# Kernel optimization log

Measured on AMD Instinct MI355X. Metric: run time of the kernel, lower is better.

## Reference

```python
import jax, jax.numpy as jnp
import numpy as np

B = 8192      # batch
E = 16        # n_experts
D = 128       # per-expert input dim (equal for all experts)
U = 256       # units
F = 256       # feature_dim (gating input)
G = 4         # n_gates
K = 6         # hard-coded top-k in the original call()
TEMP = 0.01   # hard-coded softmax temperature
LEAKY_SLOPE = 0.2  # keras leaky_relu default negative slope


def setup_inputs() -> dict:
    key = jax.random.key(0)
    ks = jax.random.split(key, 5)
    return {
        "inputs": jax.random.normal(ks[0], (B, E * D), dtype=jnp.float32),
        "feature_input": jax.random.normal(ks[1], (B, F), dtype=jnp.float32),
        # stacked per-expert kernels (equal dims -> one [E, D, U] tensor)
        "expert_kernels": jax.random.normal(ks[2], (E, D, U), dtype=jnp.float32) * 0.05,
        "expert_biases": jnp.zeros((E, U), dtype=jnp.float32),
        "gating_kernels": jax.random.normal(ks[3], (G, F, E), dtype=jnp.float32) * 0.1,
        "gating_biases": jnp.zeros((G, E), dtype=jnp.float32),
        "global_weights": jnp.ones((E,), dtype=jnp.float32),
    }


def reference(inputs, feature_input, expert_kernels, expert_biases,
              gating_kernels, gating_biases, global_weights):
    # ---- per-expert dense + bias + LeakyReLU (tf.split loop -> batched einsum) ----
    x = inputs.reshape(B, E, D)                                   # [B, E, D]
    eo = jnp.einsum('bed,edu->bue', x, expert_kernels)            # [B, U, E]
    eo = eo + expert_biases.T[None, :, :]                         # bias per expert
    expert_outputs = jax.nn.leaky_relu(eo, LEAKY_SLOPE)           # [B, U, E]

    # ---- gating: dense + bias + ReLU, scaled by global_weights ----
    g = jnp.einsum('bf,gfe->bge', feature_input, gating_kernels)  # [B, G, E]
    g = jax.nn.relu(g + gating_biases[None, :, :]) * global_weights

    # sharp softmax over experts, then top-k selection
    p = jax.nn.softmax(g / TEMP, axis=-1)                         # [B, G, E]
    top_v, top_i = jax.lax.top_k(p, K)                            # [B, G, K]

    # gather selected expert outputs: [B, G, U, K]
    sel = jnp.take_along_axis(expert_outputs[:, None, :, :],
                              top_i[:, :, None, :], axis=-1)

    # renormalize top-k values with another sharp softmax, weighted combine
    w = jax.nn.softmax(top_v / TEMP, axis=-1)                     # [B, G, K]
    out = jnp.einsum('bguk,bgk->bgu', sel, w)                     # [B, G, U]
    concat_output = out.reshape(B, G * U)                         # concat over gates
    return concat_output, expert_outputs
```

## Files before the change

### kernel.cpp

```cpp
#include <hip/hip_runtime.h>
#include <stdint.h>

#define NB 8192
#define NE 16
#define ND 128
#define NU 256
#define NF 256
#define NG 4
#define NK 6
#define ITEMP_LOG2E 144.26950408889634f

typedef short short4v __attribute__((ext_vector_type(4)));
typedef short short8v __attribute__((ext_vector_type(8)));
typedef float float4v __attribute__((ext_vector_type(4)));

__device__ __forceinline__ short f2bf(float x) {
  uint32_t u = __builtin_bit_cast(uint32_t, x);
  u += 0x7FFFu + ((u >> 16) & 1u);
  return (short)(u >> 16);
}

__global__ __launch_bounds__(256) void prep_kernel(
    const float* __restrict__ ek,
    short* __restrict__ pb)
{
  int gid = (blockIdx.x << 8) | threadIdx.x;
  int lane = gid & 63, ut = (gid >> 6) & 15, ks = (gid >> 10) & 3, e = gid >> 12;
  int krow = ks * 32 + ((lane >> 4) * 8);
  int ucol = ut * 16 + (lane & 15);
  const float* src = ek + (size_t)(e * 128 + krow) * 256 + ucol;
  short8v v;
#pragma unroll
  for (int j = 0; j < 8; ++j) v[j] = f2bf(src[(size_t)j * 256]);
  *(short8v*)(pb + (size_t)gid * 8) = v;
}

#define APITCH 2056
#define WPITCH 64

__global__ __launch_bounds__(1024, 4) void moe_kernel(
    const float* __restrict__ x,
    const float* __restrict__ feat,
    const float* __restrict__ gk,
    const float* __restrict__ gbias,
    const float* __restrict__ gw,
    const float* __restrict__ eb,
    const short* __restrict__ pb,
    float* __restrict__ out)
{
  __shared__ __align__(16) short ash[32 * APITCH];
  __shared__ __align__(16) float wsh[32 * WPITCH];
  __shared__ __align__(16) float stg[16 * 256];
  int bt = blockIdx.x, tid = threadIdx.x;
  int w = tid >> 6, lane = tid & 63;

  if (w < 14) {
    const float4v* s = (const float4v*)(x + (size_t)bt * 32 * 2048);
    for (int idx = w * 64 + lane; idx < 16384; idx += 896) {
      int row = idx >> 9;
      int colf = (idx & 511) << 2;
      float4v v = __builtin_nontemporal_load(s + idx);
      short4v sv;
      sv[0] = f2bf(v[0]); sv[1] = f2bf(v[1]); sv[2] = f2bf(v[2]); sv[3] = f2bf(v[3]);
      *(short4v*)&ash[row * APITCH + colf] = sv;
    }
  } else {
    int rb = (w - 14) * 16;
    int gate = lane >> 4, e = lane & 15;
    float gwv = gw[e];
    float bias = gbias[gate * 16 + e];
    const float* gkp = gk + (size_t)gate * (NF * NE) + e;
#pragma unroll 1
    for (int p = 0; p < 2; ++p) {
      float acc[8];
#pragma unroll
      for (int i = 0; i < 8; ++i) acc[i] = bias;
      const float* fb = feat + ((size_t)bt * 32 + rb + p * 8) * 256;
      for (int f = 0; f < NF; f += 4) {
        float g0 = gkp[(f + 0) * 16], g1 = gkp[(f + 1) * 16];
        float g2 = gkp[(f + 2) * 16], g3 = gkp[(f + 3) * 16];
#pragma unroll
        for (int i = 0; i < 8; ++i) {
          float4v fv = *(const float4v*)(fb + i * 256 + f);
          acc[i] = fmaf(fv[0], g0, acc[i]);
          acc[i] = fmaf(fv[1], g1, acc[i]);
          acc[i] = fmaf(fv[2], g2, acc[i]);
          acc[i] = fmaf(fv[3], g3, acc[i]);
        }
      }
#pragma unroll 1
      for (int i = 0; i < 8; ++i) {
        float v = acc[i] > 0.f ? acc[i] : 0.f;
        v *= gwv;
        float m = v;
#pragma unroll
        for (int off = 1; off < 16; off <<= 1) m = fmaxf(m, __shfl_xor(m, off, 16));
        float ex = exp2f((v - m) * ITEMP_LOG2E);
        float s = ex;
#pragma unroll
        for (int off = 1; off < 16; off <<= 1) s += __shfl_xor(s, off, 16);
        float pr = ex / s;
        float cur = pr;
        float topv[NK]; int topi[NK];
#pragma unroll
        for (int r = 0; r < NK; ++r) {
          float mv = cur;
#pragma unroll
          for (int off = 1; off < 16; off <<= 1) mv = fmaxf(mv, __shfl_xor(mv, off, 16));
          int cand = (cur == mv) ? e : 16;
#pragma unroll
          for (int off = 1; off < 16; off <<= 1) cand = min(cand, __shfl_xor(cand, off, 16));
          topv[r] = mv; topi[r] = cand;
          if (e == cand) cur = -1.f;
        }
        float wv[NK], wsum = 0.f;
#pragma unroll
        for (int r = 0; r < NK; ++r) {
          wv[r] = exp2f((topv[r] - topv[0]) * ITEMP_LOG2E);
          wsum += wv[r];
        }
        float inv = 1.f / wsum;
        float wdv = 0.f;
#pragma unroll
        for (int r = 0; r < NK; ++r) wdv = (topi[r] == e) ? wv[r] * inv : wdv;
        wsh[(rb + p * 8 + i) * WPITCH + lane] = wdv;
      }
    }
  }
  __syncthreads();

  int btile = w >> 3, utq = (w >> 1) & 3, th = w & 1;
  int q = lane >> 4, col = lane & 15;
  int am = lane & 15;
  float* outcat = out;
  float* outeo = out + (size_t)NB * NG * NU;
  const short8v* pbv = (const short8v*)pb;
  float* ws = stg + w * 256;
  size_t bb = (size_t)bt * 32 + btile * 16;
  int arow = (btile * 16 + am) * APITCH;
  int wrow = (btile * 16 + q * 4) * WPITCH;

  float csave[4][4];

#pragma unroll 1
  for (int tl = 0; tl < 2; ++tl) {
    int t = th * 2 + tl;
    int ut = utq * 4 + t;
    float4v acc[16];
    float4v zero = {0.f, 0.f, 0.f, 0.f};
#pragma unroll
    for (int e = 0; e < 16; ++e) acc[e] = zero;
#pragma unroll
    for (int e = 0; e < 16; ++e) {
#pragma unroll
      for (int ks = 0; ks < 4; ++ks) {
        short8v a = *(const short8v*)&ash[arow + e * 128 + ks * 32 + q * 8];
        short8v b = pbv[((e * 4 + ks) * 16 + ut) * 64 + lane];
        acc[e] = __builtin_amdgcn_mfma_f32_16x16x32_bf16(a, b, acc[e], 0, 0, 0);
      }
    }
    float v[16][4];
#pragma unroll
    for (int e = 0; e < 16; ++e) {
      float bv = eb[e * 256 + ut * 16 + col];
#pragma unroll
      for (int r = 0; r < 4; ++r) {
        float z = acc[e][r] + bv;
        v[e][r] = z > 0.f ? z : 0.2f * z;
      }
    }
#pragma unroll
    for (int r = 0; r < 4; ++r) {
#pragma unroll
      for (int qq = 0; qq < 4; ++qq) {
        if (q == qq) {
#pragma unroll
          for (int c = 0; c < 4; ++c) {
            float4v o = {v[4 * c + 0][r], v[4 * c + 1][r], v[4 * c + 2][r], v[4 * c + 3][r]};
            *(float4v*)(ws + (c * 16 + col) * 4) = o;
          }
        }
        __builtin_amdgcn_wave_barrier();
        {
          size_t b = bb + (size_t)(qq * 4 + r);
          float4v val = *(const float4v*)(ws + lane * 4);
          float* dst = outeo + b * 4096 + (size_t)ut * 256 + (lane & 15) * 16 + (lane >> 4) * 4;
          *(float4v*)dst = val;
        }
        __builtin_amdgcn_wave_barrier();
      }
    }
#pragma unroll
    for (int r = 0; r < 4; ++r) {
      size_t b = bb + (size_t)(q * 4 + r);
#pragma unroll
      for (int g = 0; g < 4; ++g) {
        float sacc = 0.f;
#pragma unroll
        for (int ec = 0; ec < 16; ec += 4) {
          float4v wv = *(const float4v*)&wsh[wrow + r * WPITCH + g * 16 + ec];
          sacc = fmaf(wv[0], v[ec][r], sacc);
          sacc = fmaf(wv[1], v[ec + 1][r], sacc);
          sacc = fmaf(wv[2], v[ec + 2][r], sacc);
          sacc = fmaf(wv[3], v[ec + 3][r], sacc);
        }
        if (tl == 0) {
          csave[r][g] = sacc;
        } else {
          float* cb = outcat + b * 1024 + g * 256 + (ut - 1) * 16 + col;
          cb[0] = csave[r][g];
          cb[16] = sacc;
        }
      }
    }
  }
}

extern "C" void kernel_launch(void* const* d_in, const int* in_sizes, int n_in,
                              void* d_out, int out_size, void* d_ws, size_t ws_size,
                              hipStream_t stream) {
  const float* x     = (const float*)d_in[0];
  const float* feat  = (const float*)d_in[1];
  const float* ek    = (const float*)d_in[2];
  const float* eb    = (const float*)d_in[3];
  const float* gk    = (const float*)d_in[4];
  const float* gbias = (const float*)d_in[5];
  const float* gw    = (const float*)d_in[6];
  float* out = (float*)d_out;
  short* pbf = (short*)d_ws;

  prep_kernel<<<256, 256, 0, stream>>>(ek, pbf);
  moe_kernel<<<256, 1024, 0, stream>>>(x, feat, gk, gbias, gw, eb, pbf, out);
}
```

Measured before the change: 325.3 us.

## Reorder packed expert weights, double-buffer B loads, batch input loads, rebalance gating waves

The prep kernel now writes bf16 expert weights ordered by unit tile first, so each wave reads a contiguous slab. The MFMA loop double-buffers these B fragments in registers, prefetching the next expert's weights while the current one computes. Input staging now uses 12 waves that each issue 11 or 10 independent nontemporal loads before converting, to raise memory-level parallelism. Gating moves to 4 waves of 8 rows each with 16-wide kernel prefetch, at the cost of more registers and a different wave balance.

```diff
diff --git a/kernel.cpp b/kernel.cpp
--- a/kernel.cpp
+++ b/kernel.cpp
@@ -32,7 +32,8 @@
   short8v v;
 #pragma unroll
   for (int j = 0; j < 8; ++j) v[j] = f2bf(src[(size_t)j * 256]);
-  *(short8v*)(pb + (size_t)gid * 8) = v;
+  size_t widx = (((size_t)ut * 16 + e) * 4 + ks) * 64 + lane;
+  *(short8v*)(pb + widx * 8) = v;
 }
 
 #define APITCH 2056
@@ -54,77 +55,103 @@
   int bt = blockIdx.x, tid = threadIdx.x;
   int w = tid >> 6, lane = tid & 63;
 
-  if (w < 14) {
+  if (w < 12) {
     const float4v* s = (const float4v*)(x + (size_t)bt * 32 * 2048);
-    for (int idx = w * 64 + lane; idx < 16384; idx += 896) {
-      int row = idx >> 9;
-      int colf = (idx & 511) << 2;
+    int base = w * 64 + lane;
+    float4v buf[11];
+#pragma unroll
+    for (int k = 0; k < 11; ++k) buf[k] = __builtin_nontemporal_load(s + base + k * 768);
+#pragma unroll
+    for (int k = 0; k < 11; ++k) {
+      int idx = base + k * 768;
+      int row = idx >> 9, colf = (idx & 511) << 2;
+      short4v sv;
+      sv[0] = f2bf(buf[k][0]); sv[1] = f2bf(buf[k][1]);
+      sv[2] = f2bf(buf[k][2]); sv[3] = f2bf(buf[k][3]);
+      *(short4v*)&ash[row * APITCH + colf] = sv;
+    }
+#pragma unroll
+    for (int k = 0; k < 10; ++k) buf[k] = __builtin_nontemporal_load(s + base + (11 + k) * 768);
+#pragma unroll
+    for (int k = 0; k < 10; ++k) {
+      int idx = base + (11 + k) * 768;
+      int row = idx >> 9, colf = (idx & 511) << 2;
+      short4v sv;
+      sv[0] = f2bf(buf[k][0]); sv[1] = f2bf(buf[k][1]);
+      sv[2] = f2bf(buf[k][2]); sv[3] = f2bf(buf[k][3]);
+      *(short4v*)&ash[row * APITCH + colf] = sv;
+    }
+    if (base < 256) {
+      int idx = base + 16128;
       float4v v = __builtin_nontemporal_load(s + idx);
+      int row = idx >> 9, colf = (idx & 511) << 2;
       short4v sv;
       sv[0] = f2bf(v[0]); sv[1] = f2bf(v[1]); sv[2] = f2bf(v[2]); sv[3] = f2bf(v[3]);
       *(short4v*)&ash[row * APITCH + colf] = sv;
     }
   } else {
-    int rb = (w - 14) * 16;
+    int rb = (w - 12) * 8;
     int gate = lane >> 4, e = lane & 15;
     float gwv = gw[e];
     float bias = gbias[gate * 16 + e];
     const float* gkp = gk + (size_t)gate * (NF * NE) + e;
+    const float* fb = feat + ((size_t)bt * 32 + rb) * 256;
+    float acc[8];
+#pragma unroll
+    for (int i = 0; i < 8; ++i) acc[i] = bias;
 #pragma unroll 1
-    for (int p = 0; p < 2; ++p) {
-      float acc[8];
-#pragma unroll
-      for (int i = 0; i < 8; ++i) acc[i] = bias;
-      const float* fb = feat + ((size_t)bt * 32 + rb + p * 8) * 256;
-      for (int f = 0; f < NF; f += 4) {
-        float g0 = gkp[(f + 0) * 16], g1 = gkp[(f + 1) * 16];
-        float g2 = gkp[(f + 2) * 16], g3 = gkp[(f + 3) * 16];
+    for (int f0 = 0; f0 < NF; f0 += 16) {
+      float gv[16];
+#pragma unroll
+      for (int j = 0; j < 16; ++j) gv[j] = gkp[(f0 + j) * 16];
+#pragma unroll
+      for (int j = 0; j < 16; j += 4) {
 #pragma unroll
         for (int i = 0; i < 8; ++i) {
-          float4v fv = *(const float4v*)(fb + i * 256 + f);
-          acc[i] = fmaf(fv[0], g0, acc[i]);
-          acc[i] = fmaf(fv[1], g1, acc[i]);
-          acc[i] = fmaf(fv[2], g2, acc[i]);
-          acc[i] = fmaf(fv[3], g3, acc[i]);
-        }
-      }
+          float4v fv = *(const float4v*)(fb + i * 256 + f0 + j);
+          acc[i] = fmaf(fv[0], gv[j + 0], acc[i]);
+          acc[i] = fmaf(fv[1], gv[j + 1], acc[i]);
+          acc[i] = fmaf(fv[2], gv[j + 2], acc[i]);
+          acc[i] = fmaf(fv[3], gv[j + 3], acc[i]);
+        }
+      }
+    }
 #pragma unroll 1
-      for (int i = 0; i < 8; ++i) {
-        float v = acc[i] > 0.f ? acc[i] : 0.f;
-        v *= gwv;
-        float m = v;
-#pragma unroll
-        for (int off = 1; off < 16; off <<= 1) m = fmaxf(m, __shfl_xor(m, off, 16));
-        float ex = exp2f((v - m) * ITEMP_LOG2E);
-        float s = ex;
-#pragma unroll
-        for (int off = 1; off < 16; off <<= 1) s += __shfl_xor(s, off, 16);
-        float pr = ex / s;
-        float cur = pr;
-        float topv[NK]; int topi[NK];
-#pragma unroll
-        for (int r = 0; r < NK; ++r) {
-          float mv = cur;
-#pragma unroll
-          for (int off = 1; off < 16; off <<= 1) mv = fmaxf(mv, __shfl_xor(mv, off, 16));
-          int cand = (cur == mv) ? e : 16;
-#pragma unroll
-          for (int off = 1; off < 16; off <<= 1) cand = min(cand, __shfl_xor(cand, off, 16));
-          topv[r] = mv; topi[r] = cand;
-          if (e == cand) cur = -1.f;
-        }
-        float wv[NK], wsum = 0.f;
-#pragma unroll
-        for (int r = 0; r < NK; ++r) {
-          wv[r] = exp2f((topv[r] - topv[0]) * ITEMP_LOG2E);
-          wsum += wv[r];
-        }
-        float inv = 1.f / wsum;
-        float wdv = 0.f;
-#pragma unroll
-        for (int r = 0; r < NK; ++r) wdv = (topi[r] == e) ? wv[r] * inv : wdv;
-        wsh[(rb + p * 8 + i) * WPITCH + lane] = wdv;
-      }
+    for (int i = 0; i < 8; ++i) {
+      float v = acc[i] > 0.f ? acc[i] : 0.f;
+      v *= gwv;
+      float m = v;
+#pragma unroll
+      for (int off = 1; off < 16; off <<= 1) m = fmaxf(m, __shfl_xor(m, off, 16));
+      float ex = exp2f((v - m) * ITEMP_LOG2E);
+      float s = ex;
+#pragma unroll
+      for (int off = 1; off < 16; off <<= 1) s += __shfl_xor(s, off, 16);
+      float pr = ex / s;
+      float cur = pr;
+      float topv[NK]; int topi[NK];
+#pragma unroll
+      for (int r = 0; r < NK; ++r) {
+        float mv = cur;
+#pragma unroll
+        for (int off = 1; off < 16; off <<= 1) mv = fmaxf(mv, __shfl_xor(mv, off, 16));
+        int cand = (cur == mv) ? e : 16;
+#pragma unroll
+        for (int off = 1; off < 16; off <<= 1) cand = min(cand, __shfl_xor(cand, off, 16));
+        topv[r] = mv; topi[r] = cand;
+        if (e == cand) cur = -1.f;
+      }
+      float wv[NK], wsum = 0.f;
+#pragma unroll
+      for (int r = 0; r < NK; ++r) {
+        wv[r] = exp2f((topv[r] - topv[0]) * ITEMP_LOG2E);
+        wsum += wv[r];
+      }
+      float inv = 1.f / wsum;
+      float wdv = 0.f;
+#pragma unroll
+      for (int r = 0; r < NK; ++r) wdv = (topi[r] == e) ? wv[r] * inv : wdv;
+      wsh[(rb + i) * WPITCH + lane] = wdv;
     }
   }
   __syncthreads();
@@ -146,17 +173,31 @@
   for (int tl = 0; tl < 2; ++tl) {
     int t = th * 2 + tl;
     int ut = utq * 4 + t;
+    const short8v* bp = pbv + (size_t)ut * 4096;
     float4v acc[16];
     float4v zero = {0.f, 0.f, 0.f, 0.f};
 #pragma unroll
     for (int e = 0; e < 16; ++e) acc[e] = zero;
-#pragma unroll
-    for (int e = 0; e < 16; ++e) {
+    short8v bA[4], bB[4];
+#pragma unroll
+    for (int ks = 0; ks < 4; ++ks) bA[ks] = bp[ks * 64 + lane];
+#pragma unroll
+    for (int e = 0; e < 16; e += 2) {
+#pragma unroll
+      for (int ks = 0; ks < 4; ++ks) bB[ks] = bp[(e + 1) * 256 + ks * 64 + lane];
 #pragma unroll
       for (int ks = 0; ks < 4; ++ks) {
         short8v a = *(const short8v*)&ash[arow + e * 128 + ks * 32 + q * 8];
-        short8v b = pbv[((e * 4 + ks) * 16 + ut) * 64 + lane];
-        acc[e] = __builtin_amdgcn_mfma_f32_16x16x32_bf16(a, b, acc[e], 0, 0, 0);
+        acc[e] = __builtin_amdgcn_mfma_f32_16x16x32_bf16(a, bA[ks], acc[e], 0, 0, 0);
+      }
+      if (e + 2 < 16) {
+#pragma unroll
+        for (int ks = 0; ks < 4; ++ks) bA[ks] = bp[(e + 2) * 256 + ks * 64 + lane];
+      }
+#pragma unroll
+      for (int ks = 0; ks < 4; ++ks) {
+        short8v a = *(const short8v*)&ash[arow + (e + 1) * 128 + ks * 32 + q * 8];
+        acc[e + 1] = __builtin_amdgcn_mfma_f32_16x16x32_bf16(a, bB[ks], acc[e + 1], 0, 0, 0);
       }
     }
     float v[16][4];
```

Measured after the change: 327.0 us. Within noise of the previous version (+0.5%).
